# Kernel tuning notes

Measured on AMD Instinct MI355X. Metric: run time of the kernel, lower is better.

The kernel has to match this reference:

```python
import jax, jax.numpy as jnp
import numpy as np

D, H, W = 96, 160, 160
N_FLOWS = 3
RANGE_FLOW = 0.4


def make_base_grid():
    # torch.meshgrid over arange per dim, stacked: [1, 3, D, H, W], channel order (d, h, w)
    zz, yy, xx = jnp.meshgrid(jnp.arange(D), jnp.arange(H), jnp.arange(W), indexing='ij')
    return jnp.stack([zz, yy, xx]).astype(jnp.float32)[None]


def normalize_grid(g):
    # g: [1,3,D,H,W] voxel coords (d,h,w). Apply 2*(v/(s-1) - 0.5), permute to
    # channels-last and reverse channel order -> (x,y,z) as grid_sample expects.
    scale = jnp.array([2.0 / (D - 1), 2.0 / (H - 1), 2.0 / (W - 1)], jnp.float32).reshape(1, 3, 1, 1, 1)
    g = g * scale - 1.0
    return jnp.moveaxis(g, 1, -1)[..., ::-1]  # [1,D,H,W,3], xyz


def grid_sample_3d(img, grid):
    # Trilinear grid_sample, align_corners=False, zeros padding (torch defaults).
    # img: [N,C,D,H,W]; grid: [N,D,H,W,3] with (x,y,z) in [-1,1].
    N, C, Di, Hi, Wi = img.shape
    x = ((grid[..., 0] + 1.0) * Wi - 1.0) * 0.5
    y = ((grid[..., 1] + 1.0) * Hi - 1.0) * 0.5
    z = ((grid[..., 2] + 1.0) * Di - 1.0) * 0.5
    x0 = jnp.floor(x); y0 = jnp.floor(y); z0 = jnp.floor(z)
    tx = x - x0; ty = y - y0; tz = z - z0
    x0i = x0.astype(jnp.int32); y0i = y0.astype(jnp.int32); z0i = z0.astype(jnp.int32)

    gather = jax.vmap(lambda im, a, b, c: im[:, a, b, c])  # per-batch [C,D,H,W] gather

    out = jnp.zeros((N, C) + x.shape[1:], img.dtype)
    for dz in (0, 1):
        for dy in (0, 1):
            for dx in (0, 1):
                xi = x0i + dx; yi = y0i + dy; zi = z0i + dz
                w = ((tx if dx else 1.0 - tx) * (ty if dy else 1.0 - ty) * (tz if dz else 1.0 - tz))
                valid = ((xi >= 0) & (xi < Wi) & (yi >= 0) & (yi < Hi) & (zi >= 0) & (zi < Di))
                xi = jnp.clip(xi, 0, Wi - 1); yi = jnp.clip(yi, 0, Hi - 1); zi = jnp.clip(zi, 0, Di - 1)
                vals = gather(img, zi, yi, xi)  # [N,C,D,H,W]
                out = out + vals * (w * valid)[:, None]
    return out


def setup_inputs() -> dict:
    key = jax.random.key(0)
    k1, k2, k3 = jax.random.split(key, 3)
    src = jax.random.normal(k1, (1, 1, D, H, W), jnp.float32)
    flow_list = jax.random.normal(k2, (N_FLOWS, 1, 3, D, H, W), jnp.float32)
    final_flow = jax.random.normal(k3, (1, 3, D, H, W), jnp.float32)
    range_flow = jnp.float32(RANGE_FLOW)
    return {"src": src, "flow_list": flow_list, "final_flow": final_flow, "range_flow": range_flow}


def reference(src, flow_list, final_flow, range_flow):
    base = make_base_grid()  # [1,3,D,H,W]
    flows = [flow_list[i] for i in range(flow_list.shape[0])] + [final_flow]
    composed = flows[0]
    warped = composed
    for dvf in flows[1:]:
        grid2 = normalize_grid(base + dvf * range_flow)
        warped = grid_sample_3d(composed, grid2)  # warp running composition by dvf
        composed = warped + dvf
    out_flow = warped + final_flow  # == final composed dvf
    new_locs = normalize_grid(base + composed * range_flow)
    deform_2_img = grid_sample_3d(src, new_locs)
    return (deform_2_img, out_flow)
```

## Files before the change

kernel.cpp:

```cpp
#include <hip/hip_runtime.h>

constexpr int Dd  = 96;
constexpr int Hh  = 160;
constexpr int Ww  = 160;
constexpr int HW  = Hh * Ww;
constexpr int DHW = Dd * HW;

__device__ __forceinline__ float remap_z(float v) { return v * ((float)Dd / (float)(Dd - 1)) - 0.5f; }
__device__ __forceinline__ float remap_y(float v) { return v * ((float)Hh / (float)(Hh - 1)) - 0.5f; }
__device__ __forceinline__ float remap_x(float v) { return v * ((float)Ww / (float)(Ww - 1)) - 0.5f; }

__device__ __forceinline__ void tri_setup(float x, float y, float z,
                                          int off[8], float wgt[8]) {
    float xf = floorf(x), yf = floorf(y), zf = floorf(z);
    float tx = x - xf, ty = y - yf, tz = z - zf;
    int x0 = (int)xf, y0 = (int)yf, z0 = (int)zf;
    float wx[2] = {1.0f - tx, tx};
    float wy[2] = {1.0f - ty, ty};
    float wz[2] = {1.0f - tz, tz};
    int k = 0;
#pragma unroll
    for (int dz = 0; dz < 2; ++dz) {
        int zi = z0 + dz;
        bool vz = (zi >= 0) && (zi < Dd);
        int zc = min(max(zi, 0), Dd - 1);
#pragma unroll
        for (int dy = 0; dy < 2; ++dy) {
            int yi = y0 + dy;
            bool vy = (yi >= 0) && (yi < Hh);
            int yc = min(max(yi, 0), Hh - 1);
#pragma unroll
            for (int dx = 0; dx < 2; ++dx) {
                int xi = x0 + dx;
                bool vx = (xi >= 0) && (xi < Ww);
                int xc = min(max(xi, 0), Ww - 1);
                float w = wz[dz] * wy[dy] * wx[dx];
                wgt[k] = (vx && vy && vz) ? w : 0.0f;
                off[k] = zc * HW + yc * Ww + xc;
                ++k;
            }
        }
    }
}

__global__ __launch_bounds__(256) void warp_compose(
        const float* __restrict__ composed,
        const float* __restrict__ dvf,
        const float* __restrict__ rf_ptr,
        float* __restrict__ out)
{
    int idx = blockIdx.x * blockDim.x + threadIdx.x;
    if (idx >= DHW) return;
    float rf = *rf_ptr;

    int d = idx / HW;
    int rem = idx - d * HW;
    int h = rem / Ww;
    int w = rem - h * Ww;

    float fd = dvf[idx];
    float fh = dvf[DHW + idx];
    float fw = dvf[2 * DHW + idx];

    float z = remap_z((float)d + fd * rf);
    float y = remap_y((float)h + fh * rf);
    float x = remap_x((float)w + fw * rf);

    int off[8]; float wgt[8];
    tri_setup(x, y, z, off, wgt);

    float a0 = 0.0f, a1 = 0.0f, a2 = 0.0f;
#pragma unroll
    for (int k = 0; k < 8; ++k) {
        float wk = wgt[k];
        int o = off[k];
        a0 += wk * composed[o];
        a1 += wk * composed[DHW + o];
        a2 += wk * composed[2 * DHW + o];
    }
    out[idx]           = a0 + fd;
    out[DHW + idx]     = a1 + fh;
    out[2 * DHW + idx] = a2 + fw;
}

__global__ __launch_bounds__(256) void warp_src(
        const float* __restrict__ src,
        const float* __restrict__ composed,
        const float* __restrict__ rf_ptr,
        float* __restrict__ out)
{
    int idx = blockIdx.x * blockDim.x + threadIdx.x;
    if (idx >= DHW) return;
    float rf = *rf_ptr;

    int d = idx / HW;
    int rem = idx - d * HW;
    int h = rem / Ww;
    int w = rem - h * Ww;

    float fd = composed[idx];
    float fh = composed[DHW + idx];
    float fw = composed[2 * DHW + idx];

    float z = remap_z((float)d + fd * rf);
    float y = remap_y((float)h + fh * rf);
    float x = remap_x((float)w + fw * rf);

    int off[8]; float wgt[8];
    tri_setup(x, y, z, off, wgt);

    float acc = 0.0f;
#pragma unroll
    for (int k = 0; k < 8; ++k) {
        acc += wgt[k] * src[off[k]];
    }
    out[idx] = acc;
}

extern "C" void kernel_launch(void* const* d_in, const int* in_sizes, int n_in,
                              void* d_out, int out_size, void* d_ws, size_t ws_size,
                              hipStream_t stream) {
    const float* src        = (const float*)d_in[0];
    const float* flow_list  = (const float*)d_in[1];
    const float* final_flow = (const float*)d_in[2];
    const float* rf         = (const float*)d_in[3];

    float* out_img  = (float*)d_out;
    float* out_flow = (float*)d_out + DHW;

    float* buf0 = (float*)d_ws;
    float* buf1 = buf0 + 3 * (size_t)DHW;

    const float* f0 = flow_list;
    const float* f1 = flow_list + 3 * (size_t)DHW;
    const float* f2 = flow_list + 6 * (size_t)DHW;

    dim3 block(256);
    dim3 grid((DHW + 255) / 256);

    warp_compose<<<grid, block, 0, stream>>>(f0, f1, rf, buf0);
    warp_compose<<<grid, block, 0, stream>>>(buf0, f2, rf, buf1);
    warp_compose<<<grid, block, 0, stream>>>(buf1, final_flow, rf, out_flow);
    warp_src<<<grid, block, 0, stream>>>(src, out_flow, rf, out_img);
}
```

Baseline: 301.6 us.

## Store intermediate composed flows as interleaved float4 for single-load trilinear gathers

Adds a pack kernel that converts the first flow into an interleaved float4 layout, and makes the compose kernels gather one float4 per corner instead of three scattered planar loads. The intermediate buffers are float4 and only the last compose writes planar output. This is meant to cut the number of scattered memory transactions in the gather-bound warps. In exchange it adds an extra launch and pass over the flow, and the padding lane means 33% more bytes per element. The grid size now relies on DHW being divisible by 256.

```diff
diff --git a/kernel.cpp b/kernel.cpp
--- a/kernel.cpp
+++ b/kernel.cpp
@@ -43,11 +43,21 @@
     }
 }
 
-__global__ __launch_bounds__(256) void warp_compose(
-        const float* __restrict__ composed,
+__global__ __launch_bounds__(256) void pack3to4(
+        const float* __restrict__ f, float4* __restrict__ out)
+{
+    int idx = blockIdx.x * blockDim.x + threadIdx.x;
+    if (idx >= DHW) return;
+    out[idx] = make_float4(f[idx], f[DHW + idx], f[2 * DHW + idx], 0.0f);
+}
+
+template <bool PLANAR_OUT>
+__global__ __launch_bounds__(256) void warp_compose4(
+        const float4* __restrict__ composed,
         const float* __restrict__ dvf,
         const float* __restrict__ rf_ptr,
-        float* __restrict__ out)
+        float* __restrict__ outp,
+        float4* __restrict__ out4)
 {
     int idx = blockIdx.x * blockDim.x + threadIdx.x;
     if (idx >= DHW) return;
@@ -72,15 +82,19 @@
     float a0 = 0.0f, a1 = 0.0f, a2 = 0.0f;
 #pragma unroll
     for (int k = 0; k < 8; ++k) {
+        float4 v = composed[off[k]];
         float wk = wgt[k];
-        int o = off[k];
-        a0 += wk * composed[o];
-        a1 += wk * composed[DHW + o];
-        a2 += wk * composed[2 * DHW + o];
+        a0 += wk * v.x;
+        a1 += wk * v.y;
+        a2 += wk * v.z;
     }
-    out[idx]           = a0 + fd;
-    out[DHW + idx]     = a1 + fh;
-    out[2 * DHW + idx] = a2 + fw;
+    if (PLANAR_OUT) {
+        outp[idx]           = a0 + fd;
+        outp[DHW + idx]     = a1 + fh;
+        outp[2 * DHW + idx] = a2 + fw;
+    } else {
+        out4[idx] = make_float4(a0 + fd, a1 + fh, a2 + fw, 0.0f);
+    }
 }
 
 __global__ __launch_bounds__(256) void warp_src(
@@ -128,18 +142,19 @@
     float* out_img  = (float*)d_out;
     float* out_flow = (float*)d_out + DHW;
 
-    float* buf0 = (float*)d_ws;
-    float* buf1 = buf0 + 3 * (size_t)DHW;
+    float4* bufA = (float4*)d_ws;
+    float4* bufB = bufA + DHW;
 
     const float* f0 = flow_list;
     const float* f1 = flow_list + 3 * (size_t)DHW;
     const float* f2 = flow_list + 6 * (size_t)DHW;
 
     dim3 block(256);
-    dim3 grid((DHW + 255) / 256);
+    dim3 grid(DHW / 256);
 
-    warp_compose<<<grid, block, 0, stream>>>(f0, f1, rf, buf0);
-    warp_compose<<<grid, block, 0, stream>>>(buf0, f2, rf, buf1);
-    warp_compose<<<grid, block, 0, stream>>>(buf1, final_flow, rf, out_flow);
+    pack3to4<<<grid, block, 0, stream>>>(f0, bufA);
+    warp_compose4<false><<<grid, block, 0, stream>>>(bufA, f1, rf, nullptr, bufB);
+    warp_compose4<false><<<grid, block, 0, stream>>>(bufB, f2, rf, nullptr, bufA);
+    warp_compose4<true><<<grid, block, 0, stream>>>(bufA, final_flow, rf, out_flow, nullptr);
     warp_src<<<grid, block, 0, stream>>>(src, out_flow, rf, out_img);
 }
```

Measured after the change: 294.5 us. 1.02x faster.
